# Performance work log

Measured on AMD Instinct MI355X. Metric: run time of the kernel, lower is better.

## Reference

```python
import jax, jax.numpy as jnp
import numpy as np
import math

D = 768
H = 12
HD = D // H  # 64
DFF = 4 * D


def _layernorm(x, g, b, eps=1e-5):
    mu = jnp.mean(x, axis=-1, keepdims=True)
    var = jnp.var(x, axis=-1, keepdims=True)
    return (x - mu) * jax.lax.rsqrt(var + eps) * g + b


def _new_gelu(x):
    c = math.sqrt(2.0 / math.pi)
    return 0.5 * x * (1.0 + jnp.tanh(c * (x + 0.044715 * x * x * x)))


def setup_inputs() -> dict:
    key = jax.random.key(0)
    ks = jax.random.split(key, 8)
    B, N = 8, 1024
    s = 0.02
    return {
        "x": jax.random.normal(ks[0], (B, N, D), jnp.float32),
        "pad_mask": jnp.ones((B, N), jnp.int32),
        "ln1_g": jnp.ones((D,), jnp.float32),
        "ln1_b": jnp.zeros((D,), jnp.float32),
        "w_attn": jax.random.normal(ks[1], (D, 3 * D), jnp.float32) * s,
        "b_attn": jnp.zeros((3 * D,), jnp.float32),
        "w_proj": jax.random.normal(ks[2], (D, D), jnp.float32) * s,
        "b_proj": jnp.zeros((D,), jnp.float32),
        "ln2_g": jnp.ones((D,), jnp.float32),
        "ln2_b": jnp.zeros((D,), jnp.float32),
        "w_fc": jax.random.normal(ks[3], (D, DFF), jnp.float32) * s,
        "b_fc": jnp.zeros((DFF,), jnp.float32),
        "w_fc2": jax.random.normal(ks[4], (DFF, D), jnp.float32) * s,
        "b_fc2": jnp.zeros((D,), jnp.float32),
    }


def reference(x, pad_mask, ln1_g, ln1_b, w_attn, b_attn, w_proj, b_proj,
              ln2_g, ln2_b, w_fc, b_fc, w_fc2, b_fc2):
    B, N, C = x.shape
    # --- attention branch (note: source's causal masked_fill is NOT in-place,
    # so the causal mask is effectively never applied; only pad_mask is) ---
    h = _layernorm(x, ln1_g, ln1_b)
    qkv = h @ w_attn + b_attn  # [B,N,3D]
    q, k, v = jnp.split(qkv, 3, axis=-1)
    q = q.reshape(B, N, H, HD).transpose(0, 2, 1, 3)  # [B,H,N,hd]
    k = k.reshape(B, N, H, HD).transpose(0, 2, 1, 3)
    v = v.reshape(B, N, H, HD).transpose(0, 2, 1, 3)
    att = jnp.einsum('bhqd,bhkd->bhqk', q, k) * (1.0 / math.sqrt(HD))
    # pad mask broadcasts as [B,1,N,1]: masks query rows where pad==0
    att = jnp.where(pad_mask[:, None, :, None] == 0, -jnp.inf, att)
    att = jax.nn.softmax(att, axis=-1)
    o = jnp.einsum('bhqk,bhkd->bhqd', att, v)
    o = o.transpose(0, 2, 1, 3).reshape(B, N, C)
    x = x + (o @ w_proj + b_proj)
    # --- MLP branch ---
    h2 = _layernorm(x, ln2_g, ln2_b)
    x = x + (_new_gelu(h2 @ w_fc + b_fc) @ w_fc2 + b_fc2)
    return x
```

## Files before the change

### kernel.cpp

```cpp
#include <hip/hip_runtime.h>
#include <hip/hip_bf16.h>

typedef __bf16 bf16;
typedef __bf16 bf16x8 __attribute__((ext_vector_type(8)));
typedef __bf16 bf16x4 __attribute__((ext_vector_type(4)));
typedef float f32x4 __attribute__((ext_vector_type(4)));

#define SEQ 1024
#define BATCH 8
#define DM 768
#define NH 12
#define HDIM 64
#define DFF 3072
#define NTOK (BATCH*SEQ)

#define AS1 __attribute__((address_space(1)))
#define AS3 __attribute__((address_space(3)))
#define MFMA16(a, b, c) __builtin_amdgcn_mfma_f32_16x16x32_bf16(a, b, c, 0, 0, 0)

__device__ __forceinline__ float gelu_f(float x) {
  const float c = 0.7978845608028654f;
  float z = c * (x + 0.044715f * x * x * x);
  return x / (1.0f + __expf(-2.0f * z));
}

__global__ __launch_bounds__(256) void transpose4_kernel(
    const float* __restrict__ in0, bf16* __restrict__ out0,
    const float* __restrict__ in1, bf16* __restrict__ out1,
    const float* __restrict__ in2, bf16* __restrict__ out2,
    const float* __restrict__ in3, bf16* __restrict__ out3) {
  __shared__ float tile[32][33];
  int id = blockIdx.x;
  const float* in; bf16* out; int R, C;
  if (id < 1728)      { in = in0; out = out0; R = 768;  C = 2304; }
  else if (id < 2304) { in = in1; out = out1; R = 768;  C = 768;  id -= 1728; }
  else if (id < 4608) { in = in2; out = out2; R = 768;  C = 3072; id -= 2304; }
  else                { in = in3; out = out3; R = 3072; C = 768;  id -= 4608; }
  int nc = C >> 5;
  int c0 = (id % nc) * 32, r0 = (id / nc) * 32;
  int tx = threadIdx.x & 31, ty = threadIdx.x >> 5;
  #pragma unroll
  for (int i = 0; i < 4; ++i)
    tile[ty + i * 8][tx] = in[(size_t)(r0 + ty + i * 8) * C + c0 + tx];
  __syncthreads();
  #pragma unroll
  for (int i = 0; i < 4; ++i)
    out[(size_t)(c0 + ty + i * 8) * R + r0 + tx] = (bf16)tile[tx][ty + i * 8];
}

__global__ __launch_bounds__(256) void ln_kernel(
    const float* __restrict__ x, const float* __restrict__ g,
    const float* __restrict__ bta, bf16* __restrict__ out) {
  int row = blockIdx.x;
  int tid = threadIdx.x;
  const float* xr = x + (size_t)row * DM;
  float v0 = xr[tid], v1 = xr[tid + 256], v2 = xr[tid + 512];
  float s1 = v0 + v1 + v2;
  float s2 = v0 * v0 + v1 * v1 + v2 * v2;
  #pragma unroll
  for (int m = 32; m >= 1; m >>= 1) {
    s1 += __shfl_xor(s1, m, 64);
    s2 += __shfl_xor(s2, m, 64);
  }
  __shared__ float ps1[4], ps2[4];
  int wid = tid >> 6;
  if ((tid & 63) == 0) { ps1[wid] = s1; ps2[wid] = s2; }
  __syncthreads();
  float t1 = ps1[0] + ps1[1] + ps1[2] + ps1[3];
  float t2 = ps2[0] + ps2[1] + ps2[2] + ps2[3];
  float mean = t1 * (1.0f / DM);
  float var = t2 * (1.0f / DM) - mean * mean;
  float rstd = rsqrtf(var + 1e-5f);
  bf16* orow = out + (size_t)row * DM;
  orow[tid]       = (bf16)((v0 - mean) * rstd * g[tid]       + bta[tid]);
  orow[tid + 256] = (bf16)((v1 - mean) * rstd * g[tid + 256] + bta[tid + 256]);
  orow[tid + 512] = (bf16)((v2 - mean) * rstd * g[tid + 512] + bta[tid + 512]);
}

__global__ __launch_bounds__(256) void ln_bf16_kernel(
    const bf16* __restrict__ x, const float* __restrict__ g,
    const float* __restrict__ bta, bf16* __restrict__ out) {
  int row = blockIdx.x;
  int tid = threadIdx.x;
  const bf16* xr = x + (size_t)row * DM;
  float v[4] = {0.f, 0.f, 0.f, 0.f};
  if (tid < 192) {
    bf16x4 q = *(const bf16x4*)(xr + tid * 4);
    #pragma unroll
    for (int j = 0; j < 4; ++j) v[j] = (float)q[j];
  }
  float s1 = (v[0] + v[1]) + (v[2] + v[3]);
  float s2 = (v[0] * v[0] + v[1] * v[1]) + (v[2] * v[2] + v[3] * v[3]);
  #pragma unroll
  for (int m = 32; m >= 1; m >>= 1) {
    s1 += __shfl_xor(s1, m, 64);
    s2 += __shfl_xor(s2, m, 64);
  }
  __shared__ float ps1[4], ps2[4];
  int wid = tid >> 6;
  if ((tid & 63) == 0) { ps1[wid] = s1; ps2[wid] = s2; }
  __syncthreads();
  float t1 = ps1[0] + ps1[1] + ps1[2] + ps1[3];
  float t2 = ps2[0] + ps2[1] + ps2[2] + ps2[3];
  float mean = t1 * (1.0f / DM);
  float var = t2 * (1.0f / DM) - mean * mean;
  float rstd = rsqrtf(var + 1e-5f);
  if (tid < 192) {
    bf16x4 o;
    #pragma unroll
    for (int j = 0; j < 4; ++j)
      o[j] = (bf16)((v[j] - mean) * rstd * g[tid * 4 + j] + bta[tid * 4 + j]);
    *(bf16x4*)(out + (size_t)row * DM + tid * 4) = o;
  }
}

__global__ __launch_bounds__(512, 4) void gemm_kernel(
    const bf16* __restrict__ A, int lda, const bf16* __restrict__ BT,
    const float* __restrict__ bias, const float* __restrict__ residF,
    const bf16* __restrict__ residB,
    float* __restrict__ outF, bf16* __restrict__ outB,
    int N, int K, int flags) {
  __shared__ bf16 As[3][128 * 32];
  __shared__ bf16 Bs[3][256 * 32];
  int tid = threadIdx.x;
  int wid = tid >> 6, lane = tid & 63;
  int nct = N >> 8;
  int nwg = gridDim.x;
  int bid = blockIdx.x;
  int lid = ((nwg & 7) == 0) ? ((bid & 7) * (nwg >> 3) + (bid >> 3)) : bid;
  int row0 = (lid / nct) * 128, col0 = (lid % nct) * 256;
  int wm = wid >> 2, wn = wid & 3;
  int fr = lane & 15, fq = lane >> 4;
  f32x4 acc[4][4] = {};

  int srow = tid >> 2;
  int ssl = ((tid & 3) ^ ((tid >> 3) & 3)) * 8;
  const bf16* gA  = A + (size_t)(row0 + srow) * lda + ssl;
  const bf16* gB  = BT + (size_t)(col0 + srow) * K + ssl;
  const bf16* gB2 = gB + (size_t)128 * K;
  int ldsA  = (wid * 16) * 32;
  int ldsB  = (wid * 16) * 32;
  int ldsB2 = (128 + wid * 16) * 32;

  int RB0 = wn * 64 + 0 * 16 + fr, RB1 = wn * 64 + 1 * 16 + fr;
  int RB2 = wn * 64 + 2 * 16 + fr, RB3 = wn * 64 + 3 * 16 + fr;
  int RA0 = wm * 64 + 0 * 16 + fr, RA1 = wm * 64 + 1 * 16 + fr;
  int RA2 = wm * 64 + 2 * 16 + fr, RA3 = wm * 64 + 3 * 16 + fr;
  int offB0 = RB0 * 32 + (fq ^ ((RB0 >> 1) & 3)) * 8;
  int offB1 = RB1 * 32 + (fq ^ ((RB1 >> 1) & 3)) * 8;
  int offB2 = RB2 * 32 + (fq ^ ((RB2 >> 1) & 3)) * 8;
  int offB3 = RB3 * 32 + (fq ^ ((RB3 >> 1) & 3)) * 8;
  int offA0 = RA0 * 32 + (fq ^ ((RA0 >> 1) & 3)) * 8;
  int offA1 = RA1 * 32 + (fq ^ ((RA1 >> 1) & 3)) * 8;
  int offA2 = RA2 * 32 + (fq ^ ((RA2 >> 1) & 3)) * 8;
  int offA3 = RA3 * 32 + (fq ^ ((RA3 >> 1) & 3)) * 8;

  int nt = K >> 5;

  __builtin_amdgcn_global_load_lds((const AS1 void*)(gA), (AS3 void*)(&As[0][ldsA]), 16, 0, 0);
  __builtin_amdgcn_global_load_lds((const AS1 void*)(gB), (AS3 void*)(&Bs[0][ldsB]), 16, 0, 0);
  __builtin_amdgcn_global_load_lds((const AS1 void*)(gB2), (AS3 void*)(&Bs[0][ldsB2]), 16, 0, 0);
  __builtin_amdgcn_global_load_lds((const AS1 void*)(gA + 32), (AS3 void*)(&As[1][ldsA]), 16, 0, 0);
  __builtin_amdgcn_global_load_lds((const AS1 void*)(gB + 32), (AS3 void*)(&Bs[1][ldsB]), 16, 0, 0);
  __builtin_amdgcn_global_load_lds((const AS1 void*)(gB2 + 32), (AS3 void*)(&Bs[1][ldsB2]), 16, 0, 0);

#define KS(CB, T)                                                              \
  {                                                                            \
    if ((T) == nt - 1) asm volatile("s_waitcnt vmcnt(0)" ::: "memory");        \
    else               asm volatile("s_waitcnt vmcnt(3)" ::: "memory");        \
    __builtin_amdgcn_s_barrier();                                              \
    bf16x8 b0 = *(const bf16x8*)&Bs[CB][offB0];                                \
    bf16x8 b1 = *(const bf16x8*)&Bs[CB][offB1];                                \
    bf16x8 b2 = *(const bf16x8*)&Bs[CB][offB2];                                \
    bf16x8 b3 = *(const bf16x8*)&Bs[CB][offB3];                                \
    bf16x8 a0 = *(const bf16x8*)&As[CB][offA0];                                \
    bf16x8 a1 = *(const bf16x8*)&As[CB][offA1];                                \
    if ((T) + 2 < nt)                                                          \
      __builtin_amdgcn_global_load_lds(                                        \
          (const AS1 void*)(gA + ((T) + 2) * 32),                              \
          (AS3 void*)(&As[((CB) + 2) % 3][ldsA]), 16, 0, 0);                   \
    __builtin_amdgcn_s_barrier();                                              \
    __builtin_amdgcn_s_setprio(1);                                             \
    acc[0][0] = MFMA16(a0, b0, acc[0][0]); acc[0][1] = MFMA16(a0, b1, acc[0][1]); \
    acc[0][2] = MFMA16(a0, b2, acc[0][2]); acc[0][3] = MFMA16(a0, b3, acc[0][3]); \
    acc[1][0] = MFMA16(a1, b0, acc[1][0]); acc[1][1] = MFMA16(a1, b1, acc[1][1]); \
    acc[1][2] = MFMA16(a1, b2, acc[1][2]); acc[1][3] = MFMA16(a1, b3, acc[1][3]); \
    __builtin_amdgcn_s_setprio(0);                                             \
    bf16x8 a2 = *(const bf16x8*)&As[CB][offA2];                                \
    bf16x8 a3 = *(const bf16x8*)&As[CB][offA3];                                \
    if ((T) + 2 < nt) {                                                        \
      __builtin_amdgcn_global_load_lds(                                        \
          (const AS1 void*)(gB + ((T) + 2) * 32),                              \
          (AS3 void*)(&Bs[((CB) + 2) % 3][ldsB]), 16, 0, 0);                   \
      __builtin_amdgcn_global_load_lds(                                        \
          (const AS1 void*)(gB2 + ((T) + 2) * 32),                             \
          (AS3 void*)(&Bs[((CB) + 2) % 3][ldsB2]), 16, 0, 0);                  \
    }                                                                          \
    __builtin_amdgcn_s_barrier();                                              \
    __builtin_amdgcn_s_setprio(1);                                             \
    acc[2][0] = MFMA16(a2, b0, acc[2][0]); acc[2][1] = MFMA16(a2, b1, acc[2][1]); \
    acc[2][2] = MFMA16(a2, b2, acc[2][2]); acc[2][3] = MFMA16(a2, b3, acc[2][3]); \
    acc[3][0] = MFMA16(a3, b0, acc[3][0]); acc[3][1] = MFMA16(a3, b1, acc[3][1]); \
    acc[3][2] = MFMA16(a3, b2, acc[3][2]); acc[3][3] = MFMA16(a3, b3, acc[3][3]); \
    __builtin_amdgcn_s_setprio(0);                                             \
  }

  for (int t = 0; t < nt; t += 3) {
    KS(0, t);
    KS(1, t + 1);
    KS(2, t + 2);
  }
#undef KS

  bool gelu = (flags & 1);
  #pragma unroll
  for (int m = 0; m < 4; ++m) {
    #pragma unroll
    for (int n = 0; n < 4; ++n) {
      int col = col0 + wn * 64 + n * 16 + fr;
      float bs = bias[col];
      #pragma unroll
      for (int r = 0; r < 4; ++r) {
        int row = row0 + wm * 64 + m * 16 + fq * 4 + r;
        float v = acc[m][n][r] + bs;
        if (gelu) v = gelu_f(v);
        if (residF) v += residF[(size_t)row * N + col];
        if (residB) v += (float)residB[(size_t)row * N + col];
        if (outF) outF[(size_t)row * N + col] = v;
        else outB[(size_t)row * N + col] = (bf16)v;
      }
    }
  }
}

__global__ __launch_bounds__(256) void vtrans_kernel(
    const bf16* __restrict__ qkv, bf16* __restrict__ vt) {
  int bh = blockIdx.y;
  int b = bh / NH, h = bh % NH;
  int n0 = blockIdx.x * 64;
  __shared__ bf16 tile[64][65];
  int tx = threadIdx.x & 63, ty = threadIdx.x >> 6;
  #pragma unroll
  for (int i = 0; i < 16; ++i) {
    int n = ty + i * 4;
    tile[tx][n] = qkv[(size_t)(b * SEQ + n0 + n) * (3 * DM) + 2 * DM + h * HDIM + tx];
  }
  __syncthreads();
  #pragma unroll
  for (int i = 0; i < 16; ++i) {
    int hd = ty + i * 4;
    vt[((size_t)bh * HDIM + hd) * SEQ + n0 + tx] = tile[hd][tx];
  }
}

__global__ __launch_bounds__(256) void attn_kernel(
    bf16* __restrict__ qkv, const bf16* __restrict__ vt,
    const int* __restrict__ pad) {
  __shared__ bf16 Ks[2][64 * 64];
  __shared__ bf16 Vs[2][64 * 64];
  __shared__ bf16 P_lds[4][16 * 72];
  int blk = blockIdx.x;
  int lblk = (blk & 7) * 192 + (blk >> 3);
  int qt = lblk & 15;
  int bh = lblk >> 4;
  int b = bh / NH, h = bh % NH;
  int tid = threadIdx.x, wid = tid >> 6, lane = tid & 63;
  int q0 = qt * 64 + wid * 16;
  int fr = lane & 15;
  int fq = lane >> 4;
  int fk = fq * 8;
  const bf16* qbase = qkv + (size_t)(b * SEQ + q0) * (3 * DM) + h * HDIM;
  bf16* Pw = &P_lds[wid][0];
  bf16x8 qf[2];
  #pragma unroll
  for (int kk = 0; kk < 2; ++kk)
    qf[kk] = *(const bf16x8*)(qbase + (size_t)fr * (3 * DM) + kk * 32 + fk);
  int srow = (wid << 4) + (lane >> 3);
  int sc = ((lane & 7) << 4) ^ ((lane >> 3) << 4);
  const bf16* kSrc = qkv + (size_t)(b * SEQ + srow) * (3 * DM) + DM + h * HDIM + (sc >> 1);
  const bf16* vSrc = vt + ((size_t)bh * HDIM + srow) * SEQ + (sc >> 1);

  auto STAGE = [&](int buf, int kt) {
    const bf16* kS = kSrc + (size_t)kt * 64 * (3 * DM);
    const bf16* vS = vSrc + kt * 64;
    bf16* kD = &Ks[buf][wid * 1024];
    bf16* vD = &Vs[buf][wid * 1024];
    __builtin_amdgcn_global_load_lds((const AS1 void*)kS, (AS3 void*)kD, 16, 0, 0);
    __builtin_amdgcn_global_load_lds((const AS1 void*)(kS + 8 * (3 * DM)), (AS3 void*)(kD + 512), 16, 0, 0);
    __builtin_amdgcn_global_load_lds((const AS1 void*)vS, (AS3 void*)vD, 16, 0, 0);
    __builtin_amdgcn_global_load_lds((const AS1 void*)(vS + 8 * SEQ), (AS3 void*)(vD + 512), 16, 0, 0);
  };

  float lp[4] = {0.f, 0.f, 0.f, 0.f};
  f32x4 oacc[4] = {};
  int padv[4];
  #pragma unroll
  for (int r = 0; r < 4; ++r) padv[r] = pad[b * SEQ + q0 + fq * 4 + r];
  bool anymask = __any(padv[0] == 0 || padv[1] == 0 || padv[2] == 0 || padv[3] == 0);
  int xr = (fr & 7) << 4;

  STAGE(0, 0);
  for (int kt = 0; kt < 16; ++kt) {
    int cur = kt & 1;
    if (kt < 15) STAGE(cur ^ 1, kt + 1);
    if (kt == 15) asm volatile("s_waitcnt vmcnt(0)" ::: "memory");
    else          asm volatile("s_waitcnt vmcnt(4)" ::: "memory");
    __builtin_amdgcn_s_barrier();

    f32x4 s[4];
    #pragma unroll
    for (int nt = 0; nt < 4; ++nt) {
      f32x4 a = {};
      #pragma unroll
      for (int kk = 0; kk < 2; ++kk) {
        int colb = (kk * 64 + fq * 16) ^ xr;
        bf16x8 kf = *(const bf16x8*)&Ks[cur][(nt * 16 + fr) * 64 + (colb >> 1)];
        a = __builtin_amdgcn_mfma_f32_16x16x32_bf16(qf[kk], kf, a, 0, 0, 0);
      }
      s[nt] = a;
    }
    if (anymask) {
      #pragma unroll
      for (int r = 0; r < 4; ++r)
        if (padv[r] == 0) { s[0][r] = 0.f; s[1][r] = 0.f; s[2][r] = 0.f; s[3][r] = 0.f; }
    }
    #pragma unroll
    for (int nt = 0; nt < 4; ++nt)
      #pragma unroll
      for (int r = 0; r < 4; ++r)
        s[nt][r] = __expf(s[nt][r] * 0.125f);
    #pragma unroll
    for (int r = 0; r < 4; ++r)
      lp[r] += (s[0][r] + s[1][r]) + (s[2][r] + s[3][r]);
    #pragma unroll
    for (int nt = 0; nt < 4; ++nt)
      #pragma unroll
      for (int r = 0; r < 4; ++r)
        Pw[(fq * 4 + r) * 72 + nt * 16 + fr] = (bf16)s[nt][r];
    #pragma unroll
    for (int nt = 0; nt < 4; ++nt) {
      #pragma unroll
      for (int ks = 0; ks < 2; ++ks) {
        bf16x8 pf = *(const bf16x8*)&Pw[fr * 72 + ks * 32 + fk];
        int colb = (ks * 64 + fq * 16) ^ xr;
        bf16x8 vf = *(const bf16x8*)&Vs[cur][(nt * 16 + fr) * 64 + (colb >> 1)];
        oacc[nt] = __builtin_amdgcn_mfma_f32_16x16x32_bf16(pf, vf, oacc[nt], 0, 0, 0);
      }
    }
    __builtin_amdgcn_s_barrier();
  }
  #pragma unroll
  for (int r = 0; r < 4; ++r) {
    float l = lp[r];
    #pragma unroll
    for (int msk = 8; msk >= 1; msk >>= 1) l += __shfl_xor(l, msk, 64);
    float inv = 1.0f / l;
    #pragma unroll
    for (int nt = 0; nt < 4; ++nt)
      qkv[(size_t)(b * SEQ + q0 + fq * 4 + r) * (3 * DM) + h * HDIM + nt * 16 + fr] =
          (bf16)(oacc[nt][r] * inv);
  }
}

extern "C" void kernel_launch(void* const* d_in, const int* in_sizes, int n_in,
                              void* d_out, int out_size, void* d_ws, size_t ws_size,
                              hipStream_t stream) {
  const float* x      = (const float*)d_in[0];
  const int*   pad    = (const int*)d_in[1];
  const float* ln1_g  = (const float*)d_in[2];
  const float* ln1_b  = (const float*)d_in[3];
  const float* w_attn = (const float*)d_in[4];
  const float* b_attn = (const float*)d_in[5];
  const float* w_proj = (const float*)d_in[6];
  const float* b_proj = (const float*)d_in[7];
  const float* ln2_g  = (const float*)d_in[8];
  const float* ln2_b  = (const float*)d_in[9];
  const float* w_fc   = (const float*)d_in[10];
  const float* b_fc   = (const float*)d_in[11];
  const float* w_fc2  = (const float*)d_in[12];
  const float* b_fc2  = (const float*)d_in[13];
  float* out = (float*)d_out;

  char* ws = (char*)d_ws;
  size_t off = 0;
  auto alloc = [&](size_t bytes) {
    void* p = ws + off;
    off += (bytes + 255) & ~(size_t)255;
    return p;
  };
  bf16* wT_attn = (bf16*)alloc((size_t)(3 * DM) * DM * 2);
  bf16* wT_proj = (bf16*)alloc((size_t)DM * DM * 2);
  bf16* wT_fc   = (bf16*)alloc((size_t)DFF * DM * 2);
  bf16* wT_fc2  = (bf16*)alloc((size_t)DM * DFF * 2);
  bf16* h       = (bf16*)alloc((size_t)NTOK * DM * 2);
  bf16* qkv     = (bf16*)alloc((size_t)NTOK * (3 * DM) * 2);
  bf16* vt      = (bf16*)alloc((size_t)BATCH * NH * HDIM * SEQ * 2);
  bf16* x1b     = (bf16*)alloc((size_t)NTOK * DM * 2);
  bf16* act     = (bf16*)alloc((size_t)NTOK * DFF * 2);

  transpose4_kernel<<<6912, 256, 0, stream>>>(
      w_attn, wT_attn, w_proj, wT_proj, w_fc, wT_fc, w_fc2, wT_fc2);
  ln_kernel<<<NTOK, 256, 0, stream>>>(x, ln1_g, ln1_b, h);
  gemm_kernel<<<576, 512, 0, stream>>>(
      h, DM, wT_attn, b_attn, nullptr, nullptr, nullptr, qkv, 3 * DM, DM, 0);
  vtrans_kernel<<<dim3(SEQ / 64, BATCH * NH), 256, 0, stream>>>(qkv, vt);
  attn_kernel<<<BATCH * NH * (SEQ / 64), 256, 0, stream>>>(qkv, vt, pad);
  gemm_kernel<<<192, 512, 0, stream>>>(
      qkv, 3 * DM, wT_proj, b_proj, x, nullptr, nullptr, x1b, DM, DM, 0);
  ln_bf16_kernel<<<NTOK, 256, 0, stream>>>(x1b, ln2_g, ln2_b, h);
  gemm_kernel<<<768, 512, 0, stream>>>(
      h, DM, wT_fc, b_fc, nullptr, nullptr, nullptr, act, DFF, DM, 1);
  gemm_kernel<<<192, 512, 0, stream>>>(
      act, DFF, wT_fc2, b_fc2, nullptr, x1b, out, nullptr, DM, DFF, 0);
}
```

Measured before the change: 303.7 us.

## Split-K the projection and FC2 GEMMs and fuse the reductions with bias, residual and LayerNorm

Adds a split-K=2 mode to the GEMM kernel. It is used for the two N=768 GEMMs (attention projection and FC2), doubling their workgroup count from 192 to 384 so more of the CUs get work. Each half of K writes its own fp32 partial result into reused scratch buffers. New reduce kernels then sum the partials and add bias and residual; the projection's reduce also applies LN2 in the same pass. The cost is a large amount of extra fp32 partial write and read traffic plus two extra launches, and the partial buffers overlap the act, h and qkv scratch regions, which are assumed dead at that point.

```diff
diff --git a/kernel.cpp b/kernel.cpp
--- a/kernel.cpp
+++ b/kernel.cpp
@@ -77,20 +77,23 @@
   orow[tid + 512] = (bf16)((v2 - mean) * rstd * g[tid + 512] + bta[tid + 512]);
 }
 
-__global__ __launch_bounds__(256) void ln_bf16_kernel(
-    const bf16* __restrict__ x, const float* __restrict__ g,
-    const float* __restrict__ bta, bf16* __restrict__ out) {
+__global__ __launch_bounds__(256) void reduce_ln_kernel(
+    const float* __restrict__ p0, const float* __restrict__ p1,
+    const float* __restrict__ bias, const float* __restrict__ resid,
+    const float* __restrict__ g, const float* __restrict__ bta,
+    bf16* __restrict__ x1b, bf16* __restrict__ h) {
   int row = blockIdx.x;
   int tid = threadIdx.x;
-  const bf16* xr = x + (size_t)row * DM;
-  float v[4] = {0.f, 0.f, 0.f, 0.f};
-  if (tid < 192) {
-    bf16x4 q = *(const bf16x4*)(xr + tid * 4);
-    #pragma unroll
-    for (int j = 0; j < 4; ++j) v[j] = (float)q[j];
-  }
-  float s1 = (v[0] + v[1]) + (v[2] + v[3]);
-  float s2 = (v[0] * v[0] + v[1] * v[1]) + (v[2] * v[2] + v[3] * v[3]);
+  size_t base = (size_t)row * DM;
+  float v0 = p0[base + tid]       + p1[base + tid]       + bias[tid]       + resid[base + tid];
+  float v1 = p0[base + tid + 256] + p1[base + tid + 256] + bias[tid + 256] + resid[base + tid + 256];
+  float v2 = p0[base + tid + 512] + p1[base + tid + 512] + bias[tid + 512] + resid[base + tid + 512];
+  bf16* xr = x1b + base;
+  xr[tid]       = (bf16)v0;
+  xr[tid + 256] = (bf16)v1;
+  xr[tid + 512] = (bf16)v2;
+  float s1 = v0 + v1 + v2;
+  float s2 = v0 * v0 + v1 * v1 + v2 * v2;
   #pragma unroll
   for (int m = 32; m >= 1; m >>= 1) {
     s1 += __shfl_xor(s1, m, 64);
@@ -105,13 +108,26 @@
   float mean = t1 * (1.0f / DM);
   float var = t2 * (1.0f / DM) - mean * mean;
   float rstd = rsqrtf(var + 1e-5f);
-  if (tid < 192) {
-    bf16x4 o;
-    #pragma unroll
-    for (int j = 0; j < 4; ++j)
-      o[j] = (bf16)((v[j] - mean) * rstd * g[tid * 4 + j] + bta[tid * 4 + j]);
-    *(bf16x4*)(out + (size_t)row * DM + tid * 4) = o;
-  }
+  bf16* orow = h + base;
+  orow[tid]       = (bf16)((v0 - mean) * rstd * g[tid]       + bta[tid]);
+  orow[tid + 256] = (bf16)((v1 - mean) * rstd * g[tid + 256] + bta[tid + 256]);
+  orow[tid + 512] = (bf16)((v2 - mean) * rstd * g[tid + 512] + bta[tid + 512]);
+}
+
+__global__ __launch_bounds__(256) void reduce_out_kernel(
+    const float* __restrict__ p0, const float* __restrict__ p1,
+    const float* __restrict__ bias, const bf16* __restrict__ resid,
+    float* __restrict__ out) {
+  int i = blockIdx.x * 256 + threadIdx.x;
+  size_t e = (size_t)i * 4;
+  f32x4 a = *(const f32x4*)(p0 + e);
+  f32x4 b = *(const f32x4*)(p1 + e);
+  f32x4 bs = *(const f32x4*)(bias + (int)(e % DM));
+  bf16x4 r = *(const bf16x4*)(resid + e);
+  f32x4 o;
+  #pragma unroll
+  for (int j = 0; j < 4; ++j) o[j] = a[j] + b[j] + bs[j] + (float)r[j];
+  *(f32x4*)(out + e) = o;
 }
 
 __global__ __launch_bounds__(512, 4) void gemm_kernel(
@@ -128,15 +144,30 @@
   int nwg = gridDim.x;
   int bid = blockIdx.x;
   int lid = ((nwg & 7) == 0) ? ((bid & 7) * (nwg >> 3) + (bid >> 3)) : bid;
-  int row0 = (lid / nct) * 128, col0 = (lid % nct) * 256;
+  int row0, col0, koff = 0, Keff = K;
+  size_t outOff = 0;
+  if (flags & 2) {
+    int half = nwg >> 1;
+    int s = lid / half;
+    int r = lid - s * half;
+    int nrt = half / nct;
+    col0 = (r / nrt) << 8;
+    row0 = (r % nrt) << 7;
+    Keff = K >> 1;
+    koff = s * Keff;
+    outOff = (size_t)s * ((size_t)nrt << 7) * (size_t)N;
+  } else {
+    row0 = (lid / nct) * 128;
+    col0 = (lid % nct) * 256;
+  }
   int wm = wid >> 2, wn = wid & 3;
   int fr = lane & 15, fq = lane >> 4;
   f32x4 acc[4][4] = {};
 
   int srow = tid >> 2;
   int ssl = ((tid & 3) ^ ((tid >> 3) & 3)) * 8;
-  const bf16* gA  = A + (size_t)(row0 + srow) * lda + ssl;
-  const bf16* gB  = BT + (size_t)(col0 + srow) * K + ssl;
+  const bf16* gA  = A + (size_t)(row0 + srow) * lda + koff + ssl;
+  const bf16* gB  = BT + (size_t)(col0 + srow) * K + koff + ssl;
   const bf16* gB2 = gB + (size_t)128 * K;
   int ldsA  = (wid * 16) * 32;
   int ldsB  = (wid * 16) * 32;
@@ -155,7 +186,7 @@
   int offA2 = RA2 * 32 + (fq ^ ((RA2 >> 1) & 3)) * 8;
   int offA3 = RA3 * 32 + (fq ^ ((RA3 >> 1) & 3)) * 8;
 
-  int nt = K >> 5;
+  int nt = Keff >> 5;
 
   __builtin_amdgcn_global_load_lds((const AS1 void*)(gA), (AS3 void*)(&As[0][ldsA]), 16, 0, 0);
   __builtin_amdgcn_global_load_lds((const AS1 void*)(gB), (AS3 void*)(&Bs[0][ldsB]), 16, 0, 0);
@@ -218,7 +249,7 @@
     #pragma unroll
     for (int n = 0; n < 4; ++n) {
       int col = col0 + wn * 64 + n * 16 + fr;
-      float bs = bias[col];
+      float bs = bias ? bias[col] : 0.f;
       #pragma unroll
       for (int r = 0; r < 4; ++r) {
         int row = row0 + wm * 64 + m * 16 + fq * 4 + r;
@@ -226,7 +257,7 @@
         if (gelu) v = gelu_f(v);
         if (residF) v += residF[(size_t)row * N + col];
         if (residB) v += (float)residB[(size_t)row * N + col];
-        if (outF) outF[(size_t)row * N + col] = v;
+        if (outF) outF[outOff + (size_t)row * N + col] = v;
         else outB[(size_t)row * N + col] = (bf16)v;
       }
     }
@@ -398,6 +429,9 @@
   bf16* x1b     = (bf16*)alloc((size_t)NTOK * DM * 2);
   bf16* act     = (bf16*)alloc((size_t)NTOK * DFF * 2);
 
+  float* partP = (float*)act;
+  float* partF = (float*)h;
+
   transpose4_kernel<<<6912, 256, 0, stream>>>(
       w_attn, wT_attn, w_proj, wT_proj, w_fc, wT_fc, w_fc2, wT_fc2);
   ln_kernel<<<NTOK, 256, 0, stream>>>(x, ln1_g, ln1_b, h);
@@ -405,11 +439,14 @@
       h, DM, wT_attn, b_attn, nullptr, nullptr, nullptr, qkv, 3 * DM, DM, 0);
   vtrans_kernel<<<dim3(SEQ / 64, BATCH * NH), 256, 0, stream>>>(qkv, vt);
   attn_kernel<<<BATCH * NH * (SEQ / 64), 256, 0, stream>>>(qkv, vt, pad);
-  gemm_kernel<<<192, 512, 0, stream>>>(
-      qkv, 3 * DM, wT_proj, b_proj, x, nullptr, nullptr, x1b, DM, DM, 0);
-  ln_bf16_kernel<<<NTOK, 256, 0, stream>>>(x1b, ln2_g, ln2_b, h);
+  gemm_kernel<<<384, 512, 0, stream>>>(
+      qkv, 3 * DM, wT_proj, nullptr, nullptr, nullptr, partP, nullptr, DM, DM, 2);
+  reduce_ln_kernel<<<NTOK, 256, 0, stream>>>(
+      partP, partP + (size_t)NTOK * DM, b_proj, x, ln2_g, ln2_b, x1b, h);
   gemm_kernel<<<768, 512, 0, stream>>>(
       h, DM, wT_fc, b_fc, nullptr, nullptr, nullptr, act, DFF, DM, 1);
-  gemm_kernel<<<192, 512, 0, stream>>>(
-      act, DFF, wT_fc2, b_fc2, nullptr, x1b, out, nullptr, DM, DFF, 0);
-}
+  gemm_kernel<<<384, 512, 0, stream>>>(
+      act, DFF, wT_fc2, nullptr, nullptr, nullptr, partF, nullptr, DM, DFF, 2);
+  reduce_out_kernel<<<(NTOK * DM) / (4 * 256), 256, 0, stream>>>(
+      partF, partF + (size_t)NTOK * DM, b_fc2, x1b, out);
+}
```

Result: faster. 290.9 us (-4.2%).
